# Kernel optimization log

Measured on AMD Instinct MI355X. Metric: run time of the kernel, lower is better.

The kernel has to match this reference:

```python
import jax, jax.numpy as jnp
import numpy as np

K = 7          # involution kernel size
P = 3          # padding = (K-1)//2
GC = 16        # group_channels in involution
EPS = 1e-5


def bn(x, g, b):
    # training-mode BatchNorm2d forward: per-channel batch stats over (B,H,W)
    m = jnp.mean(x, axis=(0, 2, 3), keepdims=True)
    v = jnp.var(x, axis=(0, 2, 3), keepdims=True)
    return (x - m) * jax.lax.rsqrt(v + EPS) * g[None, :, None, None] + b[None, :, None, None]


def conv1x1(x, w):
    # x: [B,C,H,W], w: [O,C] -> [B,O,H,W]
    return jnp.einsum('bchw,oc->bohw', x, w)


def unfold7(x):
    # torch F.unfold(kernel=7, pad=3, stride=1) -> [B, C, K*K, H, W] (C slowest, matching torch layout)
    B, C, H, W = x.shape
    xp = jnp.pad(x, ((0, 0), (0, 0), (P, P), (P, P)))
    return jnp.stack([xp[:, :, i:i + H, j:j + W] for i in range(K) for j in range(K)], axis=2)


def involution(x, wr, gr, br, ws):
    # kernel generation: 1x1 reduce -> BN -> ReLU -> 1x1 span to G*K*K per-pixel kernels
    B, C, H, W = x.shape
    G = C // GC
    t = jax.nn.relu(bn(conv1x1(x, wr), gr, br))          # [B, C//4, H, W]
    w = conv1x1(t, ws).reshape(B, G, 1, K * K, H, W)     # per-pixel kernels
    p = unfold7(x).reshape(B, G, GC, K * K, H, W)        # unfolded patches
    return jnp.sum(w * p, axis=3).reshape(B, C, H, W)    # multiply-accumulate over K*K


def setup_inputs() -> dict:
    key = jax.random.key(0)
    ks = jax.random.split(key, 14)
    Cin, Cout, mid = 256, 256, 64
    red = mid // 4                 # reduction_ratio = 4
    G = mid // GC                  # groups = 4
    s = lambda *sh: 1.0 / np.sqrt(np.prod(sh[1:]) if len(sh) > 1 else sh[0])
    return {
        'x':  jax.random.normal(ks[0], (8, Cin, 56, 56), jnp.float32),
        'w1': jax.random.normal(ks[1], (mid, Cin), jnp.float32) * s(mid, Cin),
        'g1': jnp.ones((mid,), jnp.float32),
        'b1': jnp.zeros((mid,), jnp.float32),
        'wr': jax.random.normal(ks[2], (red, mid), jnp.float32) * s(red, mid),
        'gr': jnp.ones((red,), jnp.float32),
        'br': jnp.zeros((red,), jnp.float32),
        'ws': jax.random.normal(ks[3], (K * K * G, red), jnp.float32) * s(K * K * G, red),
        'g2': jnp.ones((mid,), jnp.float32),
        'b2': jnp.zeros((mid,), jnp.float32),
        'w3': jax.random.normal(ks[4], (Cout, mid), jnp.float32) * s(Cout, mid),
        'g3': jnp.ones((Cout,), jnp.float32),
        'b3': jnp.zeros((Cout,), jnp.float32),
    }


def reference(x, w1, g1, b1, wr, gr, br, ws, g2, b2, w3, g3, b3):
    out = jax.nn.relu(bn(conv1x1(x, w1), g1, b1))        # conv1 1x1 + BN + ReLU
    out = jax.nn.relu(bn(involution(out, wr, gr, br, ws), g2, b2))  # involution + BN + ReLU
    out = bn(conv1x1(out, w3), g3, b3)                   # conv3 1x1 + BN
    return jax.nn.relu(out + x)                          # residual add + ReLU
```

## Files before the change

### kernel.cpp

```cpp
#include <hip/hip_runtime.h>

#define HW 3136
#define NPIX 25088
#define NBLK 392

#define OFF_Y1   0u
#define OFF_TR   1605632u
#define OFF_WT   2007040u
#define OFF_OUT2 6924288u
#define OFF_Y3   8529920u
#define OFF_ST   14952448u
#define ACC1 0
#define ACCR 128
#define ACC2 160
#define ACC3 288
#define FIN1 800
#define FINR 928
#define FIN2 960
#define FIN3 1088

__device__ __forceinline__ float wave_sum(float v) {
    #pragma unroll
    for (int off = 32; off > 0; off >>= 1) v += __shfl_xor(v, off, 64);
    return v;
}

__global__ __launch_bounds__(256) void k_wt(const float* __restrict__ w1,
        const float* __restrict__ w3, float* __restrict__ w1t, float* __restrict__ w3t) {
    int i = blockIdx.x * 256 + threadIdx.x;
    if (i < 16384) {
        int oc = i >> 8, ic = i & 255;
        w1t[ic * 64 + oc] = w1[i];
    } else {
        int j = i - 16384;
        int oc = j >> 6, ic = j & 63;
        w3t[ic * 256 + oc] = w3[j];
    }
}

__global__ __launch_bounds__(256, 4) void k_conv1(const float* __restrict__ x,
        const float* __restrict__ w1t, float* __restrict__ y1, float* __restrict__ st) {
    __shared__ float xs[64][64];
    __shared__ float wst[64][64];
    int t = threadIdx.x, pb = blockIdx.x;
    int b = pb / 49, hw0 = (pb % 49) * 64;
    int tx = t & 15, ty = t >> 4;
    float acc[4][4];
    #pragma unroll
    for (int i = 0; i < 4; i++)
        #pragma unroll
        for (int j = 0; j < 4; j++) acc[i][j] = 0.f;
    #pragma unroll 1
    for (int cc = 0; cc < 4; cc++) {
        #pragma unroll
        for (int i = 0; i < 16; i++) {
            int e = i * 256 + t, c = e >> 6, p = e & 63;
            xs[c][p]  = x[((b * 256) + cc * 64 + c) * HW + hw0 + p];
            wst[c][p] = w1t[(cc * 64 + c) * 64 + p];
        }
        __syncthreads();
        #pragma unroll 8
        for (int c = 0; c < 64; c++) {
            float4 xv = *(const float4*)&xs[c][tx * 4];
            float4 wv = *(const float4*)&wst[c][ty * 4];
            float xa[4] = {xv.x, xv.y, xv.z, xv.w};
            float wa[4] = {wv.x, wv.y, wv.z, wv.w};
            #pragma unroll
            for (int i = 0; i < 4; i++)
                #pragma unroll
                for (int j = 0; j < 4; j++) acc[i][j] = fmaf(wa[i], xa[j], acc[i][j]);
        }
        __syncthreads();
    }
    #pragma unroll
    for (int i = 0; i < 4; i++) {
        int oc = ty * 4 + i;
        float4 o = make_float4(acc[i][0], acc[i][1], acc[i][2], acc[i][3]);
        *(float4*)&y1[((b * 64) + oc) * HW + hw0 + tx * 4] = o;
        float s = o.x + o.y + o.z + o.w;
        float q = o.x * o.x + o.y * o.y + o.z * o.z + o.w * o.w;
        #pragma unroll
        for (int off = 1; off <= 8; off <<= 1) {
            s += __shfl_xor(s, off, 64);
            q += __shfl_xor(q, off, 64);
        }
        if (tx == 0) {
            atomicAdd(&st[ACC1 + oc], s);
            atomicAdd(&st[ACC1 + 64 + oc], q);
        }
    }
}

__global__ void k_fin(const float* __restrict__ acc, float* __restrict__ fin,
                      const float* __restrict__ gamma, const float* __restrict__ beta, int C) {
    int c = threadIdx.x;
    if (c < C) {
        float mean = acc[c] * (1.0f / (float)NPIX);
        float var  = acc[C + c] * (1.0f / (float)NPIX) - mean * mean;
        float rstd = rsqrtf(var + 1e-5f);
        float a = gamma[c] * rstd;
        fin[c] = a;
        fin[C + c] = beta[c] - mean * a;
    }
}

__global__ __launch_bounds__(256, 4) void k_bn1_convr(float* __restrict__ y1,
        const float* __restrict__ wr, float* __restrict__ tr, float* __restrict__ st) {
    __shared__ float ys[64][64];
    __shared__ float wsh[16][64];
    int t = threadIdx.x, pb = blockIdx.x;
    int b = pb / 49, hw0 = (pb % 49) * 64;
    int tx = t & 15, ty = t >> 4;
    #pragma unroll
    for (int i = 0; i < 16; i++) {
        int e = i * 256 + t, c = e >> 6, p = e & 63;
        int gi = ((b * 64) + c) * HW + hw0 + p;
        float v = y1[gi];
        v = fmaxf(st[FIN1 + c] * v + st[FIN1 + 64 + c], 0.f);
        ys[c][p] = v;
        y1[gi] = v;
    }
    #pragma unroll
    for (int i = 0; i < 4; i++) {
        int e = i * 256 + t;
        wsh[e >> 6][e & 63] = wr[e];
    }
    __syncthreads();
    float a0 = 0.f, a1 = 0.f, a2 = 0.f, a3 = 0.f;
    #pragma unroll 8
    for (int c = 0; c < 64; c++) {
        float4 yv = *(const float4*)&ys[c][tx * 4];
        float wv = wsh[ty][c];
        a0 = fmaf(wv, yv.x, a0); a1 = fmaf(wv, yv.y, a1);
        a2 = fmaf(wv, yv.z, a2); a3 = fmaf(wv, yv.w, a3);
    }
    *(float4*)&tr[((b * 16) + ty) * HW + hw0 + tx * 4] = make_float4(a0, a1, a2, a3);
    float s = a0 + a1 + a2 + a3;
    float q = a0 * a0 + a1 * a1 + a2 * a2 + a3 * a3;
    #pragma unroll
    for (int off = 1; off <= 8; off <<= 1) {
        s += __shfl_xor(s, off, 64);
        q += __shfl_xor(q, off, 64);
    }
    if (tx == 0) {
        atomicAdd(&st[ACCR + ty], s);
        atomicAdd(&st[ACCR + 16 + ty], q);
    }
}

__global__ __launch_bounds__(256) void k_invol(const float* __restrict__ y1r,
        const float* __restrict__ tr, const float* __restrict__ wsp,
        float* __restrict__ out2, float* __restrict__ st) {
    __shared__ float ts[16][256];
    __shared__ float sw[49][16];
    __shared__ float ps[16][10][64];
    __shared__ float red[4][32];
    int t = threadIdx.x, bidx = blockIdx.x;
    int ht = bidx % 14;
    int bg = bidx / 14;
    int g = bg & 3, b = bg >> 2;
    int h0 = ht * 4;
    #pragma unroll
    for (int i = 0; i < 16; i++) {
        int e = i * 256 + t, c = e >> 8, p = e & 255;
        if (p < 224) {
            float v = tr[((b * 16) + c) * HW + h0 * 56 + p];
            ts[c][p] = fmaxf(st[FINR + c] * v + st[FINR + 16 + c], 0.f);
        }
    }
    for (int e = t; e < 784; e += 256) sw[e >> 4][e & 15] = wsp[g * 784 + e];
    for (int e = t; e < 10240; e += 256) {
        int c = e / 640, r = (e >> 6) % 10, wc = e & 63;
        int gh = h0 + r - 3, gw = wc - 3;
        float v = 0.f;
        if (gh >= 0 && gh < 56 && gw >= 0 && gw < 56)
            v = y1r[((b * 64) + g * 16 + c) * HW + gh * 56 + gw];
        ps[c][r][wc] = v;
    }
    __syncthreads();
    float accv[16];
    #pragma unroll
    for (int c = 0; c < 16; c++) accv[c] = 0.f;
    bool active = t < 224;
    if (active) {
        int lh = t / 56, lw = t % 56;
        float tsr[16];
        #pragma unroll
        for (int c = 0; c < 16; c++) tsr[c] = ts[c][t];
        float kr[49];
        #pragma unroll
        for (int k = 0; k < 49; k++) {
            const float4* swr = (const float4*)&sw[k][0];
            float4 u0 = swr[0], u1 = swr[1], u2 = swr[2], u3 = swr[3];
            float v = u0.x * tsr[0];
            v = fmaf(u0.y, tsr[1], v);  v = fmaf(u0.z, tsr[2], v);  v = fmaf(u0.w, tsr[3], v);
            v = fmaf(u1.x, tsr[4], v);  v = fmaf(u1.y, tsr[5], v);  v = fmaf(u1.z, tsr[6], v);
            v = fmaf(u1.w, tsr[7], v);  v = fmaf(u2.x, tsr[8], v);  v = fmaf(u2.y, tsr[9], v);
            v = fmaf(u2.z, tsr[10], v); v = fmaf(u2.w, tsr[11], v); v = fmaf(u3.x, tsr[12], v);
            v = fmaf(u3.y, tsr[13], v); v = fmaf(u3.z, tsr[14], v); v = fmaf(u3.w, tsr[15], v);
            kr[k] = v;
        }
        #pragma unroll
        for (int k = 0; k < 49; k++) {
            int ki = k / 7, kj = k % 7;
            float kv = kr[k];
            #pragma unroll
            for (int c = 0; c < 16; c++)
                accv[c] = fmaf(kv, ps[c][lh + ki][lw + kj], accv[c]);
        }
        int hw = h0 * 56 + t;
        #pragma unroll
        for (int c = 0; c < 16; c++)
            out2[((b * 64) + g * 16 + c) * HW + hw] = accv[c];
    }
    int wave = t >> 6, lane = t & 63;
    #pragma unroll
    for (int c = 0; c < 16; c++) {
        float v = active ? accv[c] : 0.f;
        float s  = wave_sum(v);
        float s2 = wave_sum(v * v);
        if (lane == 0) { red[wave][c] = s; red[wave][16 + c] = s2; }
    }
    __syncthreads();
    if (t < 32) {
        float s = red[0][t] + red[1][t] + red[2][t] + red[3][t];
        atomicAdd(&st[ACC2 + (t >> 4) * 64 + g * 16 + (t & 15)], s);
    }
}

__global__ __launch_bounds__(256, 4) void k_bn2_conv3(const float* __restrict__ out2,
        const float* __restrict__ w3t, float* __restrict__ y3, float* __restrict__ st) {
    __shared__ float os[64][64];
    __shared__ float wst[64][64];
    int t = threadIdx.x, blk = blockIdx.x;
    int occ = blk & 3, pb = blk >> 2;
    int b = pb / 49, hw0 = (pb % 49) * 64;
    int tx = t & 15, ty = t >> 4;
    #pragma unroll
    for (int i = 0; i < 16; i++) {
        int e = i * 256 + t, c = e >> 6, p = e & 63;
        float v = out2[((b * 64) + c) * HW + hw0 + p];
        os[c][p] = fmaxf(st[FIN2 + c] * v + st[FIN2 + 64 + c], 0.f);
        wst[c][p] = w3t[c * 256 + occ * 64 + p];
    }
    __syncthreads();
    float acc[4][4];
    #pragma unroll
    for (int i = 0; i < 4; i++)
        #pragma unroll
        for (int j = 0; j < 4; j++) acc[i][j] = 0.f;
    #pragma unroll 8
    for (int c = 0; c < 64; c++) {
        float4 xv = *(const float4*)&os[c][tx * 4];
        float4 wv = *(const float4*)&wst[c][ty * 4];
        float xa[4] = {xv.x, xv.y, xv.z, xv.w};
        float wa[4] = {wv.x, wv.y, wv.z, wv.w};
        #pragma unroll
        for (int i = 0; i < 4; i++)
            #pragma unroll
            for (int j = 0; j < 4; j++) acc[i][j] = fmaf(wa[i], xa[j], acc[i][j]);
    }
    #pragma unroll
    for (int i = 0; i < 4; i++) {
        int oc = occ * 64 + ty * 4 + i;
        float4 o = make_float4(acc[i][0], acc[i][1], acc[i][2], acc[i][3]);
        *(float4*)&y3[((b * 256) + oc) * HW + hw0 + tx * 4] = o;
        float s = o.x + o.y + o.z + o.w;
        float q = o.x * o.x + o.y * o.y + o.z * o.z + o.w * o.w;
        #pragma unroll
        for (int off = 1; off <= 8; off <<= 1) {
            s += __shfl_xor(s, off, 64);
            q += __shfl_xor(q, off, 64);
        }
        if (tx == 0) {
            atomicAdd(&st[ACC3 + oc], s);
            atomicAdd(&st[ACC3 + 256 + oc], q);
        }
    }
}

__global__ __launch_bounds__(256) void k_final(const float* __restrict__ y3,
        const float* __restrict__ x, float* __restrict__ out, const float* __restrict__ st) {
    int idx = blockIdx.x * 256 + threadIdx.x;
    if (idx < 1605632) {
        int c = (idx / 784) & 255;
        float a = st[FIN3 + c], bb = st[FIN3 + 256 + c];
        float4 v  = ((const float4*)y3)[idx];
        float4 xv = ((const float4*)x)[idx];
        float4 o;
        o.x = fmaxf(a * v.x + bb + xv.x, 0.f);
        o.y = fmaxf(a * v.y + bb + xv.y, 0.f);
        o.z = fmaxf(a * v.z + bb + xv.z, 0.f);
        o.w = fmaxf(a * v.w + bb + xv.w, 0.f);
        ((float4*)out)[idx] = o;
    }
}

extern "C" void kernel_launch(void* const* d_in, const int* in_sizes, int n_in,
                              void* d_out, int out_size, void* d_ws, size_t ws_size,
                              hipStream_t stream) {
    const float* x   = (const float*)d_in[0];
    const float* w1  = (const float*)d_in[1];
    const float* g1  = (const float*)d_in[2];
    const float* b1  = (const float*)d_in[3];
    const float* wr  = (const float*)d_in[4];
    const float* gr  = (const float*)d_in[5];
    const float* br  = (const float*)d_in[6];
    const float* wsp = (const float*)d_in[7];
    const float* g2  = (const float*)d_in[8];
    const float* b2  = (const float*)d_in[9];
    const float* w3  = (const float*)d_in[10];
    const float* g3  = (const float*)d_in[11];
    const float* b3  = (const float*)d_in[12];
    float* out = (float*)d_out;
    float* w   = (float*)d_ws;
    float* y1   = w + OFF_Y1;
    float* tr   = w + OFF_TR;
    float* w1t  = w + OFF_WT;
    float* w3t  = w + OFF_WT + 16384;
    float* out2 = w + OFF_OUT2;
    float* y3   = w + OFF_Y3;
    float* st   = w + OFF_ST;

    hipMemsetAsync(st, 0, 2048 * sizeof(float), stream);
    k_wt<<<128, 256, 0, stream>>>(w1, w3, w1t, w3t);
    k_conv1<<<NBLK, 256, 0, stream>>>(x, w1t, y1, st);
    k_fin<<<1, 64, 0, stream>>>(st + ACC1, st + FIN1, g1, b1, 64);
    k_bn1_convr<<<NBLK, 256, 0, stream>>>(y1, wr, tr, st);
    k_fin<<<1, 64, 0, stream>>>(st + ACCR, st + FINR, gr, br, 16);
    k_invol<<<448, 256, 0, stream>>>(y1, tr, wsp, out2, st);
    k_fin<<<1, 64, 0, stream>>>(st + ACC2, st + FIN2, g2, b2, 64);
    k_bn2_conv3<<<NBLK * 4, 256, 0, stream>>>(out2, w3t, y3, st);
    k_fin<<<1, 256, 0, stream>>>(st + ACC3, st + FIN3, g3, b3, 256);
    k_final<<<6272, 256, 0, stream>>>(y3, x, out, st);
}
```

Baseline: 296.0 us.

## Split conv1 and involution kernels across output-channel halves for more blocks

```diff
diff --git a/kernel.cpp b/kernel.cpp
--- a/kernel.cpp
+++ b/kernel.cpp
@@ -38,44 +38,36 @@
     }
 }
 
-__global__ __launch_bounds__(256, 4) void k_conv1(const float* __restrict__ x,
+__global__ __launch_bounds__(256, 2) void k_conv1(const float* __restrict__ x,
         const float* __restrict__ w1t, float* __restrict__ y1, float* __restrict__ st) {
-    __shared__ float xs[64][64];
-    __shared__ float wst[64][64];
-    int t = threadIdx.x, pb = blockIdx.x;
+    __shared__ float ws[256][32];
+    int t = threadIdx.x, blk = blockIdx.x;
+    int oh = blk & 1, pb = blk >> 1;
     int b = pb / 49, hw0 = (pb % 49) * 64;
     int tx = t & 15, ty = t >> 4;
-    float acc[4][4];
-    #pragma unroll
-    for (int i = 0; i < 4; i++)
-        #pragma unroll
-        for (int j = 0; j < 4; j++) acc[i][j] = 0.f;
-    #pragma unroll 1
-    for (int cc = 0; cc < 4; cc++) {
-        #pragma unroll
-        for (int i = 0; i < 16; i++) {
-            int e = i * 256 + t, c = e >> 6, p = e & 63;
-            xs[c][p]  = x[((b * 256) + cc * 64 + c) * HW + hw0 + p];
-            wst[c][p] = w1t[(cc * 64 + c) * 64 + p];
-        }
-        __syncthreads();
-        #pragma unroll 8
-        for (int c = 0; c < 64; c++) {
-            float4 xv = *(const float4*)&xs[c][tx * 4];
-            float4 wv = *(const float4*)&wst[c][ty * 4];
-            float xa[4] = {xv.x, xv.y, xv.z, xv.w};
-            float wa[4] = {wv.x, wv.y, wv.z, wv.w};
-            #pragma unroll
-            for (int i = 0; i < 4; i++)
-                #pragma unroll
-                for (int j = 0; j < 4; j++) acc[i][j] = fmaf(wa[i], xa[j], acc[i][j]);
-        }
-        __syncthreads();
-    }
-    #pragma unroll
-    for (int i = 0; i < 4; i++) {
-        int oc = ty * 4 + i;
-        float4 o = make_float4(acc[i][0], acc[i][1], acc[i][2], acc[i][3]);
+    #pragma unroll
+    for (int i = 0; i < 8; i++) {
+        int e = i * 256 + t;
+        int ic = e >> 3, c4 = e & 7;
+        *(float4*)&ws[ic][c4 * 4] = *(const float4*)&w1t[ic * 64 + oh * 32 + c4 * 4];
+    }
+    __syncthreads();
+    float a00 = 0.f, a01 = 0.f, a02 = 0.f, a03 = 0.f;
+    float a10 = 0.f, a11 = 0.f, a12 = 0.f, a13 = 0.f;
+    const float* xp = x + (size_t)b * 256 * HW + hw0 + tx * 4;
+    #pragma unroll 8
+    for (int ic = 0; ic < 256; ic++) {
+        float4 xv = *(const float4*)(xp + (size_t)ic * HW);
+        float2 wv = *(const float2*)&ws[ic][ty * 2];
+        a00 = fmaf(wv.x, xv.x, a00); a01 = fmaf(wv.x, xv.y, a01);
+        a02 = fmaf(wv.x, xv.z, a02); a03 = fmaf(wv.x, xv.w, a03);
+        a10 = fmaf(wv.y, xv.x, a10); a11 = fmaf(wv.y, xv.y, a11);
+        a12 = fmaf(wv.y, xv.z, a12); a13 = fmaf(wv.y, xv.w, a13);
+    }
+    #pragma unroll
+    for (int io = 0; io < 2; io++) {
+        int oc = oh * 32 + ty * 2 + io;
+        float4 o = io ? make_float4(a10, a11, a12, a13) : make_float4(a00, a01, a02, a03);
         *(float4*)&y1[((b * 64) + oc) * HW + hw0 + tx * 4] = o;
         float s = o.x + o.y + o.z + o.w;
         float q = o.x * o.x + o.y * o.y + o.z * o.z + o.w * o.w;
@@ -153,13 +145,15 @@
         float* __restrict__ out2, float* __restrict__ st) {
     __shared__ float ts[16][256];
     __shared__ float sw[49][16];
-    __shared__ float ps[16][10][64];
-    __shared__ float red[4][32];
+    __shared__ float ps[8][10][64];
+    __shared__ float red[4][16];
     int t = threadIdx.x, bidx = blockIdx.x;
-    int ht = bidx % 14;
-    int bg = bidx / 14;
+    int h = bidx & 1, r2 = bidx >> 1;
+    int ht = r2 % 14;
+    int bg = r2 / 14;
     int g = bg & 3, b = bg >> 2;
     int h0 = ht * 4;
+    int c0 = h * 8;
     #pragma unroll
     for (int i = 0; i < 16; i++) {
         int e = i * 256 + t, c = e >> 8, p = e & 255;
@@ -169,18 +163,20 @@
         }
     }
     for (int e = t; e < 784; e += 256) sw[e >> 4][e & 15] = wsp[g * 784 + e];
-    for (int e = t; e < 10240; e += 256) {
-        int c = e / 640, r = (e >> 6) % 10, wc = e & 63;
+    for (int i = 0; i < 20; i++) {
+        int e = i * 256 + t;
+        int c = e / 640, rem = e - c * 640;
+        int r = rem >> 6, wc = rem & 63;
         int gh = h0 + r - 3, gw = wc - 3;
         float v = 0.f;
         if (gh >= 0 && gh < 56 && gw >= 0 && gw < 56)
-            v = y1r[((b * 64) + g * 16 + c) * HW + gh * 56 + gw];
+            v = y1r[((b * 64) + g * 16 + c0 + c) * HW + gh * 56 + gw];
         ps[c][r][wc] = v;
     }
     __syncthreads();
-    float accv[16];
-    #pragma unroll
-    for (int c = 0; c < 16; c++) accv[c] = 0.f;
+    float accv[8];
+    #pragma unroll
+    for (int c = 0; c < 8; c++) accv[c] = 0.f;
     bool active = t < 224;
     if (active) {
         int lh = t / 56, lw = t % 56;
@@ -205,26 +201,27 @@
             int ki = k / 7, kj = k % 7;
             float kv = kr[k];
             #pragma unroll
-            for (int c = 0; c < 16; c++)
+            for (int c = 0; c < 8; c++)
                 accv[c] = fmaf(kv, ps[c][lh + ki][lw + kj], accv[c]);
         }
         int hw = h0 * 56 + t;
         #pragma unroll
-        for (int c = 0; c < 16; c++)
-            out2[((b * 64) + g * 16 + c) * HW + hw] = accv[c];
+        for (int c = 0; c < 8; c++)
+            out2[((b * 64) + g * 16 + c0 + c) * HW + hw] = accv[c];
     }
     int wave = t >> 6, lane = t & 63;
     #pragma unroll
-    for (int c = 0; c < 16; c++) {
+    for (int c = 0; c < 8; c++) {
         float v = active ? accv[c] : 0.f;
         float s  = wave_sum(v);
         float s2 = wave_sum(v * v);
-        if (lane == 0) { red[wave][c] = s; red[wave][16 + c] = s2; }
-    }
-    __syncthreads();
-    if (t < 32) {
+        if (lane == 0) { red[wave][c] = s; red[wave][8 + c] = s2; }
+    }
+    __syncthreads();
+    if (t < 16) {
         float s = red[0][t] + red[1][t] + red[2][t] + red[3][t];
-        atomicAdd(&st[ACC2 + (t >> 4) * 64 + g * 16 + (t & 15)], s);
+        int c = t & 7, isq = t >> 3;
+        atomicAdd(&st[ACC2 + isq * 64 + g * 16 + c0 + c], s);
     }
 }
 
@@ -324,11 +321,11 @@
 
     hipMemsetAsync(st, 0, 2048 * sizeof(float), stream);
     k_wt<<<128, 256, 0, stream>>>(w1, w3, w1t, w3t);
-    k_conv1<<<NBLK, 256, 0, stream>>>(x, w1t, y1, st);
+    k_conv1<<<NBLK * 2, 256, 0, stream>>>(x, w1t, y1, st);
     k_fin<<<1, 64, 0, stream>>>(st + ACC1, st + FIN1, g1, b1, 64);
     k_bn1_convr<<<NBLK, 256, 0, stream>>>(y1, wr, tr, st);
     k_fin<<<1, 64, 0, stream>>>(st + ACCR, st + FINR, gr, br, 16);
-    k_invol<<<448, 256, 0, stream>>>(y1, tr, wsp, out2, st);
+    k_invol<<<896, 256, 0, stream>>>(y1, tr, wsp, out2, st);
     k_fin<<<1, 64, 0, stream>>>(st + ACC2, st + FIN2, g2, b2, 64);
     k_bn2_conv3<<<NBLK * 4, 256, 0, stream>>>(out2, w3t, y3, st);
     k_fin<<<1, 256, 0, stream>>>(st + ACC3, st + FIN3, g3, b3, 256);
```

Measured after the change: 293.3 us. No clear change (-0.9%).
